# Kernel tuning notes

Hardware: AMD Instinct MI355X
Metric: run time of the kernel (lower is better)

Reference implementation:

```python
import jax, jax.numpy as jnp
import numpy as np

F = 32  # node channels (both convs)


def ecc_conv(x, src, dst, e, fgn_w, fgn_b, root, bias):
    """Edge-conditioned conv: per-edge kernel from edge feats, gather-matmul-scatter."""
    n_nodes = x.shape[0]
    n_edges = e.shape[0]
    f_in = x.shape[1]
    # filter-generating network: (E, S) -> (E, F_in*F_out) -> (E, F_in, F_out)
    kernels = (e @ fgn_w + fgn_b).reshape(n_edges, f_in, F)
    # gather source node feats, per-edge matmul
    messages = jnp.einsum('ef,efo->eo', x[src], kernels)
    # scatter-sum to target nodes
    agg = jax.ops.segment_sum(messages, dst, num_segments=n_nodes)
    return jax.nn.relu(agg + x @ root + bias)


def setup_inputs() -> dict:
    key = jax.random.key(0)
    ks = jax.random.split(key, 12)
    N, E, S = 50000, 200000, 16
    s = 0.05  # small init scale to keep activations bounded through relu
    return {
        'x': jax.random.normal(ks[0], (N, F), jnp.float32),
        'e': jax.random.normal(ks[1], (E, S), jnp.float32),
        'src': jax.random.randint(ks[2], (E,), 0, N, jnp.int32),
        'dst': jax.random.randint(ks[3], (E,), 0, N, jnp.int32),
        'fgn_w1': jax.random.normal(ks[4], (S, F * F), jnp.float32) * s,
        'fgn_b1': jnp.zeros((F * F,), jnp.float32),
        'root1': jax.random.normal(ks[5], (F, F), jnp.float32) * s,
        'bias1': jnp.zeros((F,), jnp.float32),
        'fgn_w2': jax.random.normal(ks[6], (S, F * F), jnp.float32) * s,
        'fgn_b2': jnp.zeros((F * F,), jnp.float32),
        'root2': jax.random.normal(ks[7], (F, F), jnp.float32) * s,
        'bias2': jnp.zeros((F,), jnp.float32),
        'dense_w': jax.random.normal(ks[8], (F, 1), jnp.float32) * s,
        'dense_b': jnp.zeros((1,), jnp.float32),
    }


def reference(x, e, src, dst, fgn_w1, fgn_b1, root1, bias1,
              fgn_w2, fgn_b2, root2, bias2, dense_w, dense_b):
    h = ecc_conv(x, src, dst, e, fgn_w1, fgn_b1, root1, bias1)
    h = ecc_conv(h, src, dst, e, fgn_w2, fgn_b2, root2, bias2)
    pooled = jnp.sum(h, axis=0)          # global sum pool over nodes -> (F,)
    return pooled @ dense_w + dense_b    # (1,)
```

## Files before the change

### kernel.cpp

```cpp
#include <hip/hip_runtime.h>
#include <hip/hip_bf16.h>

#define F 32
#define S 16

typedef short v8s __attribute__((ext_vector_type(8)));
typedef float v4f __attribute__((ext_vector_type(4)));

__device__ __forceinline__ float bf_lo(unsigned u) { return __uint_as_float(u << 16); }
__device__ __forceinline__ float bf_hi(unsigned u) { return __uint_as_float(u & 0xffff0000u); }
__device__ __forceinline__ unsigned short f2bf(float f) {
    __hip_bfloat16 h = __float2bfloat16(f);
    return *(unsigned short*)&h;
}
__device__ __forceinline__ unsigned pack2(float a, float b) {
    return (unsigned)f2bf(a) | ((unsigned)f2bf(b) << 16);
}
static inline size_t align256(size_t b) { return (b + 255) & ~(size_t)255; }

__global__ __launch_bounds__(256) void convert_w2(
    const float* __restrict__ w1, const float* __restrict__ b1, const float* __restrict__ r1,
    const float* __restrict__ w2, const float* __restrict__ b2, const float* __restrict__ r2,
    unsigned short* __restrict__ Wf1, unsigned short* __restrict__ Wf2,
    unsigned short* __restrict__ Rt1, unsigned short* __restrict__ Rt2)
{
    const int PER = 34 * 512 + 32 * 32;
    int tid = blockIdx.x * blockDim.x + threadIdx.x;
    if (tid >= 2 * PER) return;
    const int layer = tid / PER;
    const int rem   = tid % PER;
    const float* w = layer ? w2 : w1;
    const float* b = layer ? b2 : b1;
    const float* r = layer ? r2 : r1;
    if (rem < 34 * 512) {
        const int fi   = rem >> 9;
        const int rr   = rem & 511;
        const int lane = rr >> 3;
        const int j    = rr & 7;
        const int half = fi & 1;
        const int ck   = fi >> 1;
        const int o    = (half << 4) | (lane & 15);
        const int k    = ck * 32 + (lane >> 4) * 8 + j;
        const int s    = k >> 5, f = k & 31;
        const float v  = (s < S) ? w[s * (F * F) + f * F + o] : b[f * F + o];
        (layer ? Wf2 : Wf1)[rem] = f2bf(v);
    } else {
        const int q = rem - 34 * 512;
        const int o = q >> 5, f = q & 31;
        (layer ? Rt2 : Rt1)[o * F + f] = f2bf(r[f * F + o]);
    }
}

__global__ __launch_bounds__(256) void hist_kernel(
    const int* __restrict__ dst, int* __restrict__ cnt, int E)
{
    int e = blockIdx.x * blockDim.x + threadIdx.x;
    if (e < E) atomicAdd(&cnt[dst[e]], 1);
}

__global__ __launch_bounds__(256) void scan_partial(
    const int* __restrict__ cnt, int* __restrict__ partial, int N)
{
    const int i = blockIdx.x * 256 + threadIdx.x;
    int v = (i < N) ? cnt[i] : 0;
    #pragma unroll
    for (int off = 32; off > 0; off >>= 1) v += __shfl_down(v, off, 64);
    __shared__ int wsum[4];
    const int wave = threadIdx.x >> 6, lane = threadIdx.x & 63;
    if (lane == 0) wsum[wave] = v;
    __syncthreads();
    if (threadIdx.x == 0)
        partial[blockIdx.x] = wsum[0] + wsum[1] + wsum[2] + wsum[3];
}

__global__ void scan_top(int* __restrict__ partial, int M)
{
    const int t = threadIdx.x;
    int carry = 0;
    for (int base = 0; base < M; base += 64) {
        const int i = base + t;
        const int v0 = (i < M) ? partial[i] : 0;
        int v = v0;
        #pragma unroll
        for (int off = 1; off < 64; off <<= 1) {
            int u = __shfl_up(v, off, 64);
            if (t >= off) v += u;
        }
        if (i < M) partial[i] = carry + (v - v0);
        carry += __shfl(v, 63, 64);
    }
}

__global__ __launch_bounds__(256) void scan_final(
    const int* __restrict__ cnt, const int* __restrict__ partial,
    int* __restrict__ cursor, int* __restrict__ rowptr, int N)
{
    const int i = blockIdx.x * 256 + threadIdx.x;
    const int v0 = (i < N) ? cnt[i] : 0;
    int v = v0;
    const int wave = threadIdx.x >> 6, lane = threadIdx.x & 63;
    #pragma unroll
    for (int off = 1; off < 64; off <<= 1) {
        int u = __shfl_up(v, off, 64);
        if (lane >= off) v += u;
    }
    __shared__ int wsum[4];
    if (lane == 63) wsum[wave] = v;
    __syncthreads();
    int woff = 0;
    for (int ww = 0; ww < 4; ++ww) woff += (ww < wave) ? wsum[ww] : 0;
    if (i < N) {
        const int excl = partial[blockIdx.x] + woff + (v - v0);
        cursor[i] = excl;
        rowptr[i] = excl;
    }
}

__global__ __launch_bounds__(256) void scatter_kernel(
    const int* __restrict__ dst, int* __restrict__ cursor,
    int* __restrict__ perm, int E)
{
    int e = blockIdx.x * blockDim.x + threadIdx.x;
    if (e < E) {
        int p = atomicAdd(&cursor[dst[e]], 1);
        perm[p] = e;
    }
}

__global__ __launch_bounds__(256) void esort_kernel(
    const float* __restrict__ ef, const int* __restrict__ src,
    const int* __restrict__ perm,
    float* __restrict__ ef_s, int* __restrict__ src_s, int E)
{
    const int gid = blockIdx.x * blockDim.x + threadIdx.x;
    const int slot = gid >> 2;
    if (slot >= E) return;
    const int q = gid & 3;
    const int e = perm[slot];
    ((float4*)(ef_s + (size_t)slot * S))[q] = ((const float4*)(ef + (size_t)e * S))[q];
    if (q == 0) src_s[slot] = src[e];
}

__global__ __launch_bounds__(256) void edge_msg(
    const float* __restrict__ xin,
    const float* __restrict__ ef_s,
    const int* __restrict__ src_s,
    const unsigned short* __restrict__ Wf,
    unsigned short* __restrict__ msg,
    int E)
{
    __shared__ v8s Wl[34 * 64];
    const int tid  = threadIdx.x;
    const int w    = tid >> 6;
    const int lane = tid & 63;
    const int lid  = lane & 15;
    const int quad = lane >> 4;

    {
        const uint4* s = (const uint4*)Wf;
        uint4* d = (uint4*)Wl;
        #pragma unroll
        for (int i = 0; i < 9; ++i) {
            const int idx = tid + 256 * i;
            if (idx < 2176) d[idx] = s[idx];
        }
    }
    __syncthreads();

    const int nTiles = (E + 15) >> 4;
    for (int tile = blockIdx.x * 4 + w; tile < nTiles; tile += gridDim.x * 4) {
        const int  slot = tile * 16 + lid;
        const bool live = (slot < E);
        const int  s    = live ? slot : 0;
        const int  sn   = src_s[s];
        const float4* xp = (const float4*)(xin + (size_t)sn * F + quad * 8);
        const float4 xv0 = xp[0], xv1 = xp[1];
        const float4* efv = (const float4*)(ef_s + (size_t)s * S);
        const float4 c0 = efv[0], c1 = efv[1], c2 = efv[2], c3 = efv[3];
        const float cs[S] = {c0.x, c0.y, c0.z, c0.w, c1.x, c1.y, c1.z, c1.w,
                             c2.x, c2.y, c2.z, c2.w, c3.x, c3.y, c3.z, c3.w};

        v4f acc0 = {0.f, 0.f, 0.f, 0.f};
        v4f acc1 = {0.f, 0.f, 0.f, 0.f};

        #pragma unroll
        for (int ck = 0; ck < S; ++ck) {
            const float sc = cs[ck];
            union { v8s s8; uint4 u4; } fr;
            fr.u4.x = pack2(sc * xv0.x, sc * xv0.y);
            fr.u4.y = pack2(sc * xv0.z, sc * xv0.w);
            fr.u4.z = pack2(sc * xv1.x, sc * xv1.y);
            fr.u4.w = pack2(sc * xv1.z, sc * xv1.w);
            acc0 = __builtin_amdgcn_mfma_f32_16x16x32_bf16(Wl[(2 * ck) * 64 + lane],     fr.s8, acc0, 0, 0, 0);
            acc1 = __builtin_amdgcn_mfma_f32_16x16x32_bf16(Wl[(2 * ck + 1) * 64 + lane], fr.s8, acc1, 0, 0, 0);
        }
        {
            union { v8s s8; uint4 u4; } fr;
            fr.u4.x = pack2(xv0.x, xv0.y);
            fr.u4.y = pack2(xv0.z, xv0.w);
            fr.u4.z = pack2(xv1.x, xv1.y);
            fr.u4.w = pack2(xv1.z, xv1.w);
            acc0 = __builtin_amdgcn_mfma_f32_16x16x32_bf16(Wl[32 * 64 + lane], fr.s8, acc0, 0, 0, 0);
            acc1 = __builtin_amdgcn_mfma_f32_16x16x32_bf16(Wl[33 * 64 + lane], fr.s8, acc1, 0, 0, 0);
        }

        if (live) {
            unsigned short* mp = msg + (size_t)slot * 32;
            uint2 p0, p1;
            p0.x = pack2(acc0[0], acc0[1]);
            p0.y = pack2(acc0[2], acc0[3]);
            p1.x = pack2(acc1[0], acc1[1]);
            p1.y = pack2(acc1[2], acc1[3]);
            *(uint2*)(mp + quad * 4)      = p0;
            *(uint2*)(mp + 16 + quad * 4) = p1;
        }
    }
}

__global__ __launch_bounds__(256) void rootsum(
    const float* __restrict__ in,
    const unsigned short* __restrict__ msg,
    const int* __restrict__ rowptr,
    const int* __restrict__ cnt,
    const unsigned short* __restrict__ Rt,
    const float* __restrict__ bias,
    float* __restrict__ h,
    int N)
{
    __shared__ float acc[64 * 33];
    __shared__ unsigned short As[64 * F];
    const int tid  = threadIdx.x;
    const int n0   = blockIdx.x * 64;
    const int w    = tid >> 6;
    const int lane = tid & 63;
    const int lid  = lane & 15;
    const int quad = lane >> 4;

    {
        const int nl = tid >> 2;
        const int kq = tid & 3;
        int n = n0 + nl; if (n > N - 1) n = N - 1;
        const float4* xp = (const float4*)(in + (size_t)n * F + kq * 8);
        float4 v0 = xp[0], v1 = xp[1];
        uint4 pk;
        pk.x = pack2(v0.x, v0.y);
        pk.y = pack2(v0.z, v0.w);
        pk.z = pack2(v1.x, v1.y);
        pk.w = pack2(v1.z, v1.w);
        const int slot = ((nl >> 4) * 4 + kq) * 16 + (nl & 15);
        *(uint4*)(As + slot * 8) = pk;
    }

    {
        const int nl = tid >> 2;
        const int oq = tid & 3;
        const int n  = n0 + nl;
        float a[8];
        #pragma unroll
        for (int j = 0; j < 8; ++j) a[j] = 0.f;
        if (n < N) {
            const int k0 = rowptr[n];
            const int k1 = k0 + cnt[n];
            for (int k = k0; k < k1; ++k) {
                const uint4 q = *(const uint4*)(msg + (size_t)k * 32 + oq * 8);
                a[0] += bf_lo(q.x); a[1] += bf_hi(q.x);
                a[2] += bf_lo(q.y); a[3] += bf_hi(q.y);
                a[4] += bf_lo(q.z); a[5] += bf_hi(q.z);
                a[6] += bf_lo(q.w); a[7] += bf_hi(q.w);
            }
        }
        float* ap = acc + nl * 33 + oq * 8;
        #pragma unroll
        for (int j = 0; j < 8; ++j) ap[j] = a[j];
    }
    __syncthreads();

    const int jt  = w & 1;
    const int ns0 = (w >> 1) * 2;
    const v8s rf = *(const v8s*)(Rt + (size_t)(jt * 16 + lid) * F + quad * 8);
    const int o0 = jt * 16 + quad * 4;
    const float4 bs = *(const float4*)(bias + o0);

    #pragma unroll
    for (int i = 0; i < 2; ++i) {
        const int ns = ns0 + i;
        const v8s af = *(const v8s*)(As + (((ns * 4 + quad) * 16) + lid) * 8);
        v4f d = {0.f, 0.f, 0.f, 0.f};
        d = __builtin_amdgcn_mfma_f32_16x16x32_bf16(rf, af, d, 0, 0, 0);
        const int n = n0 + ns * 16 + lid;
        if (n < N) {
            const float* ap = acc + (ns * 16 + lid) * 33 + o0;
            float4 hv;
            hv.x = fmaxf(d[0] + ap[0] + bs.x, 0.f);
            hv.y = fmaxf(d[1] + ap[1] + bs.y, 0.f);
            hv.z = fmaxf(d[2] + ap[2] + bs.z, 0.f);
            hv.w = fmaxf(d[3] + ap[3] + bs.w, 0.f);
            *(float4*)(h + (size_t)n * F + o0) = hv;
        }
    }
}

__global__ __launch_bounds__(256) void pool_kernel(
    const float* __restrict__ h, float* __restrict__ pooled, int N)
{
    const int c = threadIdx.x & (F - 1);
    const int rowsPerBlock = 256 / F;
    float p = 0.0f;
    for (int n = blockIdx.x * rowsPerBlock + (threadIdx.x >> 5);
         n < N; n += gridDim.x * rowsPerBlock)
        p += h[(size_t)n * F + c];
    __shared__ float red[256];
    red[threadIdx.x] = p;
    __syncthreads();
    for (int off = 128; off >= F; off >>= 1) {
        if (threadIdx.x < off) red[threadIdx.x] += red[threadIdx.x + off];
        __syncthreads();
    }
    if (threadIdx.x < F) atomicAdd(&pooled[threadIdx.x], red[threadIdx.x]);
}

__global__ void final_kernel(
    const float* __restrict__ pooled, const float* __restrict__ dw,
    const float* __restrict__ db, float* __restrict__ out)
{
    const int o = threadIdx.x;
    float v = (o < F) ? pooled[o] * dw[o] : 0.0f;
    #pragma unroll
    for (int off = 32; off > 0; off >>= 1) v += __shfl_down(v, off, 64);
    if (o == 0) out[0] = v + db[0];
}

__global__ __launch_bounds__(256, 2) void ecc_edge_slow(
    const float* __restrict__ x, const float* __restrict__ ef,
    const int* __restrict__ src, const int* __restrict__ dst,
    const float* __restrict__ W, const float* __restrict__ B,
    float* __restrict__ agg, int E)
{
    const int tid = blockIdx.x * blockDim.x + threadIdx.x;
    const bool live = (tid < E);
    const int e = live ? tid : (E - 1);
    const int sn = src[e], dn = dst[e];
    float xr[F];
    const float4* xp = (const float4*)(x + (size_t)sn * F);
    #pragma unroll
    for (int i = 0; i < F / 4; ++i) {
        float4 v = xp[i];
        xr[4*i+0] = v.x; xr[4*i+1] = v.y; xr[4*i+2] = v.z; xr[4*i+3] = v.w;
    }
    float acc[F];
    #pragma unroll
    for (int o = 0; o < F; ++o) acc[o] = 0.0f;
    const float* erow = ef + (size_t)e * S;
    for (int s = 0; s < S; ++s) {
        const float es = erow[s];
        const float* Ws = W + s * (F * F);
        #pragma unroll
        for (int f = 0; f < F; ++f) {
            const float z = es * xr[f];
            #pragma unroll
            for (int o = 0; o < F; ++o) acc[o] = fmaf(z, Ws[f * F + o], acc[o]);
        }
    }
    #pragma unroll
    for (int f = 0; f < F; ++f) {
        const float xf = xr[f];
        #pragma unroll
        for (int o = 0; o < F; ++o) acc[o] = fmaf(xf, B[f * F + o], acc[o]);
    }
    if (live) {
        float* ap = agg + (size_t)dn * F;
        #pragma unroll
        for (int o = 0; o < F; ++o) atomicAdd(ap + o, acc[o]);
    }
}

__global__ __launch_bounds__(256) void ecc_node_slow(
    const float* __restrict__ xin, const float* __restrict__ root,
    const float* __restrict__ bias, float* __restrict__ h, int N)
{
    int t = blockIdx.x * blockDim.x + threadIdx.x;
    if (t >= N * F) return;
    const int n = t >> 5, o = t & (F - 1);
    const float* xrow = xin + (size_t)n * F;
    float v = h[t] + bias[o];
    #pragma unroll
    for (int f = 0; f < F; ++f) v = fmaf(xrow[f], root[f * F + o], v);
    h[t] = fmaxf(v, 0.0f);
}

extern "C" void kernel_launch(void* const* d_in, const int* in_sizes, int n_in,
                              void* d_out, int out_size, void* d_ws, size_t ws_size,
                              hipStream_t stream) {
    const float* x      = (const float*)d_in[0];
    const float* efeat  = (const float*)d_in[1];
    const int*   src    = (const int*)d_in[2];
    const int*   dst    = (const int*)d_in[3];
    const float* fgn_w1 = (const float*)d_in[4];
    const float* fgn_b1 = (const float*)d_in[5];
    const float* root1  = (const float*)d_in[6];
    const float* bias1  = (const float*)d_in[7];
    const float* fgn_w2 = (const float*)d_in[8];
    const float* fgn_b2 = (const float*)d_in[9];
    const float* root2  = (const float*)d_in[10];
    const float* bias2  = (const float*)d_in[11];
    const float* dense_w = (const float*)d_in[12];
    const float* dense_b = (const float*)d_in[13];

    const int N = in_sizes[0] / F;
    const int E = in_sizes[2];

    const int gridP = (N + 255) / 256;

    const size_t pooledB = 256;
    const size_t cntB    = align256((size_t)N * 4);
    const size_t rowB    = align256((size_t)N * 4);
    const size_t curB    = align256((size_t)N * 4);
    const size_t partB   = align256((size_t)gridP * 4);
    const size_t permB   = align256((size_t)E * 4);
    const size_t efsB    = align256((size_t)E * S * 4);
    const size_t srcsB   = align256((size_t)E * 4);
    const size_t msgB    = align256((size_t)E * 32 * 2);
    const size_t hB      = (size_t)N * F * 4;
    const size_t wfB     = align256((size_t)34 * 512 * 2);
    const size_t rtB     = align256((size_t)32 * 32 * 2);

    const size_t offCnt  = pooledB;
    const size_t offRow  = offCnt + cntB;
    const size_t offCur  = offRow + rowB;
    const size_t offPart = offCur + curB;
    const size_t offPerm = offPart + partB;
    const size_t offEfs  = offPerm + permB;
    const size_t offSrcs = offEfs + efsB;
    const size_t offMsg  = offSrcs + srcsB;
    const size_t offH1   = offMsg + msgB;
    const size_t offH2   = offH1 + hB;
    const size_t offW1   = offH2 + hB;
    const size_t offW2   = offW1 + wfB;
    const size_t offR1   = offW2 + wfB;
    const size_t offR2   = offR1 + rtB;
    const size_t need    = offR2 + rtB;

    const int eB         = (E + 255) / 256;
    const int nodeBlocks = (N * F + 255) / 256;

    if (ws_size >= need) {
        float* pooled = (float*)d_ws;
        int* cnt     = (int*)((char*)d_ws + offCnt);
        int* rowptr  = (int*)((char*)d_ws + offRow);
        int* cursor  = (int*)((char*)d_ws + offCur);
        int* partial = (int*)((char*)d_ws + offPart);
        int* perm    = (int*)((char*)d_ws + offPerm);
        float* ef_s  = (float*)((char*)d_ws + offEfs);
        int*   src_s = (int*)((char*)d_ws + offSrcs);
        unsigned short* msg = (unsigned short*)((char*)d_ws + offMsg);
        float* h1    = (float*)((char*)d_ws + offH1);
        float* h2    = (float*)((char*)d_ws + offH2);
        unsigned short* Wf1 = (unsigned short*)((char*)d_ws + offW1);
        unsigned short* Wf2 = (unsigned short*)((char*)d_ws + offW2);
        unsigned short* Rt1 = (unsigned short*)((char*)d_ws + offR1);
        unsigned short* Rt2 = (unsigned short*)((char*)d_ws + offR2);

        hipMemsetAsync(d_ws, 0, pooledB + cntB, stream);

        convert_w2<<<(2 * 18432 + 255) / 256, 256, 0, stream>>>(
            fgn_w1, fgn_b1, root1, fgn_w2, fgn_b2, root2, Wf1, Wf2, Rt1, Rt2);

        hist_kernel   <<<eB, 256, 0, stream>>>(dst, cnt, E);
        scan_partial  <<<gridP, 256, 0, stream>>>(cnt, partial, N);
        scan_top      <<<1, 64, 0, stream>>>(partial, gridP);
        scan_final    <<<gridP, 256, 0, stream>>>(cnt, partial, cursor, rowptr, N);
        scatter_kernel<<<eB, 256, 0, stream>>>(dst, cursor, perm, E);
        esort_kernel  <<<(E * 4 + 255) / 256, 256, 0, stream>>>(efeat, src, perm, ef_s, src_s, E);

        const int nTiles     = (E + 15) / 16;
        int edgeBlocks = (nTiles + 3) / 4;
        if (edgeBlocks > 1024) edgeBlocks = 1024;
        const int rsBlocks   = (N + 63) / 64;

        edge_msg<<<edgeBlocks, 256, 0, stream>>>(x, ef_s, src_s, Wf1, msg, E);
        rootsum <<<rsBlocks, 256, 0, stream>>>(x, msg, rowptr, cnt, Rt1, bias1, h1, N);

        edge_msg<<<edgeBlocks, 256, 0, stream>>>(h1, ef_s, src_s, Wf2, msg, E);
        rootsum <<<rsBlocks, 256, 0, stream>>>(h1, msg, rowptr, cnt, Rt2, bias2, h2, N);

        pool_kernel <<<512, 256, 0, stream>>>(h2, pooled, N);
        final_kernel<<<1, 64, 0, stream>>>(pooled, dense_w, dense_b, (float*)d_out);
    } else {
        float* agg1   = (float*)d_ws;
        float* agg2   = agg1 + (size_t)N * F;
        float* pooled = agg2 + (size_t)N * F;
        hipMemsetAsync(d_ws, 0, (2 * (size_t)N * F + F) * sizeof(float), stream);
        ecc_edge_slow<<<eB, 256, 0, stream>>>(x, efeat, src, dst, fgn_w1, fgn_b1, agg1, E);
        ecc_node_slow<<<nodeBlocks, 256, 0, stream>>>(x, root1, bias1, agg1, N);
        ecc_edge_slow<<<eB, 256, 0, stream>>>(agg1, efeat, src, dst, fgn_w2, fgn_b2, agg2, E);
        ecc_node_slow<<<nodeBlocks, 256, 0, stream>>>(agg1, root2, bias2, agg2, N);
        pool_kernel <<<512, 256, 0, stream>>>(agg2, pooled, N);
        final_kernel<<<1, 64, 0, stream>>>(pooled, dense_w, dense_b, (float*)d_out);
    }
}
```

Baseline: 203.0 us.

## Fuse edge message MFMA with node aggregation and root transform per node block

```diff
diff --git a/kernel.cpp b/kernel.cpp
--- a/kernel.cpp
+++ b/kernel.cpp
@@ -129,8 +129,9 @@
 
 __global__ __launch_bounds__(256) void esort_kernel(
     const float* __restrict__ ef, const int* __restrict__ src,
-    const int* __restrict__ perm,
-    float* __restrict__ ef_s, int* __restrict__ src_s, int E)
+    const int* __restrict__ dst, const int* __restrict__ perm,
+    float* __restrict__ ef_s, int* __restrict__ src_s, int* __restrict__ dst_s,
+    int E)
 {
     const int gid = blockIdx.x * blockDim.x + threadIdx.x;
     const int slot = gid >> 2;
@@ -139,94 +140,22 @@
     const int e = perm[slot];
     ((float4*)(ef_s + (size_t)slot * S))[q] = ((const float4*)(ef + (size_t)e * S))[q];
     if (q == 0) src_s[slot] = src[e];
-}
-
-__global__ __launch_bounds__(256) void edge_msg(
-    const float* __restrict__ xin,
+    if (q == 1) dst_s[slot] = dst[e];
+}
+
+__global__ __launch_bounds__(256) void ecc_fused(
+    const float* __restrict__ in,
     const float* __restrict__ ef_s,
     const int* __restrict__ src_s,
+    const int* __restrict__ dst_s,
+    const int* __restrict__ rowptr,
     const unsigned short* __restrict__ Wf,
-    unsigned short* __restrict__ msg,
-    int E)
-{
-    __shared__ v8s Wl[34 * 64];
-    const int tid  = threadIdx.x;
-    const int w    = tid >> 6;
-    const int lane = tid & 63;
-    const int lid  = lane & 15;
-    const int quad = lane >> 4;
-
-    {
-        const uint4* s = (const uint4*)Wf;
-        uint4* d = (uint4*)Wl;
-        #pragma unroll
-        for (int i = 0; i < 9; ++i) {
-            const int idx = tid + 256 * i;
-            if (idx < 2176) d[idx] = s[idx];
-        }
-    }
-    __syncthreads();
-
-    const int nTiles = (E + 15) >> 4;
-    for (int tile = blockIdx.x * 4 + w; tile < nTiles; tile += gridDim.x * 4) {
-        const int  slot = tile * 16 + lid;
-        const bool live = (slot < E);
-        const int  s    = live ? slot : 0;
-        const int  sn   = src_s[s];
-        const float4* xp = (const float4*)(xin + (size_t)sn * F + quad * 8);
-        const float4 xv0 = xp[0], xv1 = xp[1];
-        const float4* efv = (const float4*)(ef_s + (size_t)s * S);
-        const float4 c0 = efv[0], c1 = efv[1], c2 = efv[2], c3 = efv[3];
-        const float cs[S] = {c0.x, c0.y, c0.z, c0.w, c1.x, c1.y, c1.z, c1.w,
-                             c2.x, c2.y, c2.z, c2.w, c3.x, c3.y, c3.z, c3.w};
-
-        v4f acc0 = {0.f, 0.f, 0.f, 0.f};
-        v4f acc1 = {0.f, 0.f, 0.f, 0.f};
-
-        #pragma unroll
-        for (int ck = 0; ck < S; ++ck) {
-            const float sc = cs[ck];
-            union { v8s s8; uint4 u4; } fr;
-            fr.u4.x = pack2(sc * xv0.x, sc * xv0.y);
-            fr.u4.y = pack2(sc * xv0.z, sc * xv0.w);
-            fr.u4.z = pack2(sc * xv1.x, sc * xv1.y);
-            fr.u4.w = pack2(sc * xv1.z, sc * xv1.w);
-            acc0 = __builtin_amdgcn_mfma_f32_16x16x32_bf16(Wl[(2 * ck) * 64 + lane],     fr.s8, acc0, 0, 0, 0);
-            acc1 = __builtin_amdgcn_mfma_f32_16x16x32_bf16(Wl[(2 * ck + 1) * 64 + lane], fr.s8, acc1, 0, 0, 0);
-        }
-        {
-            union { v8s s8; uint4 u4; } fr;
-            fr.u4.x = pack2(xv0.x, xv0.y);
-            fr.u4.y = pack2(xv0.z, xv0.w);
-            fr.u4.z = pack2(xv1.x, xv1.y);
-            fr.u4.w = pack2(xv1.z, xv1.w);
-            acc0 = __builtin_amdgcn_mfma_f32_16x16x32_bf16(Wl[32 * 64 + lane], fr.s8, acc0, 0, 0, 0);
-            acc1 = __builtin_amdgcn_mfma_f32_16x16x32_bf16(Wl[33 * 64 + lane], fr.s8, acc1, 0, 0, 0);
-        }
-
-        if (live) {
-            unsigned short* mp = msg + (size_t)slot * 32;
-            uint2 p0, p1;
-            p0.x = pack2(acc0[0], acc0[1]);
-            p0.y = pack2(acc0[2], acc0[3]);
-            p1.x = pack2(acc1[0], acc1[1]);
-            p1.y = pack2(acc1[2], acc1[3]);
-            *(uint2*)(mp + quad * 4)      = p0;
-            *(uint2*)(mp + 16 + quad * 4) = p1;
-        }
-    }
-}
-
-__global__ __launch_bounds__(256) void rootsum(
-    const float* __restrict__ in,
-    const unsigned short* __restrict__ msg,
-    const int* __restrict__ rowptr,
-    const int* __restrict__ cnt,
     const unsigned short* __restrict__ Rt,
     const float* __restrict__ bias,
     float* __restrict__ h,
-    int N)
-{
+    int N, int E)
+{
+    __shared__ v8s Wl[34 * 64];
     __shared__ float acc[64 * 33];
     __shared__ unsigned short As[64 * F];
     const int tid  = threadIdx.x;
@@ -236,6 +165,17 @@
     const int lid  = lane & 15;
     const int quad = lane >> 4;
 
+    {
+        const uint4* s = (const uint4*)Wf;
+        uint4* d = (uint4*)Wl;
+        #pragma unroll
+        for (int i = 0; i < 9; ++i) {
+            const int idx = tid + 256 * i;
+            if (idx < 2176) d[idx] = s[idx];
+        }
+    }
+    #pragma unroll
+    for (int i = tid; i < 64 * 33; i += 256) acc[i] = 0.f;
     {
         const int nl = tid >> 2;
         const int kq = tid & 3;
@@ -250,28 +190,52 @@
         const int slot = ((nl >> 4) * 4 + kq) * 16 + (nl & 15);
         *(uint4*)(As + slot * 8) = pk;
     }
-
-    {
-        const int nl = tid >> 2;
-        const int oq = tid & 3;
-        const int n  = n0 + nl;
-        float a[8];
-        #pragma unroll
-        for (int j = 0; j < 8; ++j) a[j] = 0.f;
-        if (n < N) {
-            const int k0 = rowptr[n];
-            const int k1 = k0 + cnt[n];
-            for (int k = k0; k < k1; ++k) {
-                const uint4 q = *(const uint4*)(msg + (size_t)k * 32 + oq * 8);
-                a[0] += bf_lo(q.x); a[1] += bf_hi(q.x);
-                a[2] += bf_lo(q.y); a[3] += bf_hi(q.y);
-                a[4] += bf_lo(q.z); a[5] += bf_hi(q.z);
-                a[6] += bf_lo(q.w); a[7] += bf_hi(q.w);
-            }
-        }
-        float* ap = acc + nl * 33 + oq * 8;
-        #pragma unroll
-        for (int j = 0; j < 8; ++j) ap[j] = a[j];
+    __syncthreads();
+
+    const int half = w & 1;
+    const int k0   = rowptr[n0];
+    const int kEnd = (n0 + 64 < N) ? rowptr[n0 + 64] : E;
+
+    for (int k = k0 + (w >> 1) * 16; k < kEnd; k += 32) {
+        const int  slot = k + lid;
+        const bool live = (slot < kEnd);
+        const int  sl   = live ? slot : k;
+        const int  sn   = src_s[sl];
+        const int  dn   = dst_s[sl];
+        const float4* xp = (const float4*)(in + (size_t)sn * F + quad * 8);
+        const float4 xv0 = xp[0], xv1 = xp[1];
+        const float4* efv = (const float4*)(ef_s + (size_t)sl * S);
+        const float4 c0 = efv[0], c1 = efv[1], c2 = efv[2], c3 = efv[3];
+        const float cs[S] = {c0.x, c0.y, c0.z, c0.w, c1.x, c1.y, c1.z, c1.w,
+                             c2.x, c2.y, c2.z, c2.w, c3.x, c3.y, c3.z, c3.w};
+
+        v4f a = {0.f, 0.f, 0.f, 0.f};
+        #pragma unroll
+        for (int ck = 0; ck < S; ++ck) {
+            const float sc = cs[ck];
+            union { v8s s8; uint4 u4; } fr;
+            fr.u4.x = pack2(sc * xv0.x, sc * xv0.y);
+            fr.u4.y = pack2(sc * xv0.z, sc * xv0.w);
+            fr.u4.z = pack2(sc * xv1.x, sc * xv1.y);
+            fr.u4.w = pack2(sc * xv1.z, sc * xv1.w);
+            a = __builtin_amdgcn_mfma_f32_16x16x32_bf16(Wl[(2 * ck + half) * 64 + lane], fr.s8, a, 0, 0, 0);
+        }
+        {
+            union { v8s s8; uint4 u4; } fr;
+            fr.u4.x = pack2(xv0.x, xv0.y);
+            fr.u4.y = pack2(xv0.z, xv0.w);
+            fr.u4.z = pack2(xv1.x, xv1.y);
+            fr.u4.w = pack2(xv1.z, xv1.w);
+            a = __builtin_amdgcn_mfma_f32_16x16x32_bf16(Wl[(32 + half) * 64 + lane], fr.s8, a, 0, 0, 0);
+        }
+
+        if (live) {
+            float* ap = acc + (dn - n0) * 33 + half * 16 + quad * 4;
+            atomicAdd(ap + 0, a[0]);
+            atomicAdd(ap + 1, a[1]);
+            atomicAdd(ap + 2, a[2]);
+            atomicAdd(ap + 3, a[3]);
+        }
     }
     __syncthreads();
 
@@ -419,7 +383,7 @@
     const size_t permB   = align256((size_t)E * 4);
     const size_t efsB    = align256((size_t)E * S * 4);
     const size_t srcsB   = align256((size_t)E * 4);
-    const size_t msgB    = align256((size_t)E * 32 * 2);
+    const size_t dstsB   = align256((size_t)E * 4);
     const size_t hB      = (size_t)N * F * 4;
     const size_t wfB     = align256((size_t)34 * 512 * 2);
     const size_t rtB     = align256((size_t)32 * 32 * 2);
@@ -431,8 +395,8 @@
     const size_t offPerm = offPart + partB;
     const size_t offEfs  = offPerm + permB;
     const size_t offSrcs = offEfs + efsB;
-    const size_t offMsg  = offSrcs + srcsB;
-    const size_t offH1   = offMsg + msgB;
+    const size_t offDsts = offSrcs + srcsB;
+    const size_t offH1   = offDsts + dstsB;
     const size_t offH2   = offH1 + hB;
     const size_t offW1   = offH2 + hB;
     const size_t offW2   = offW1 + wfB;
@@ -452,7 +416,7 @@
         int* perm    = (int*)((char*)d_ws + offPerm);
         float* ef_s  = (float*)((char*)d_ws + offEfs);
         int*   src_s = (int*)((char*)d_ws + offSrcs);
-        unsigned short* msg = (unsigned short*)((char*)d_ws + offMsg);
+        int*   dst_s = (int*)((char*)d_ws + offDsts);
         float* h1    = (float*)((char*)d_ws + offH1);
         float* h2    = (float*)((char*)d_ws + offH2);
         unsigned short* Wf1 = (unsigned short*)((char*)d_ws + offW1);
@@ -470,18 +434,15 @@
         scan_top      <<<1, 64, 0, stream>>>(partial, gridP);
         scan_final    <<<gridP, 256, 0, stream>>>(cnt, partial, cursor, rowptr, N);
         scatter_kernel<<<eB, 256, 0, stream>>>(dst, cursor, perm, E);
-        esort_kernel  <<<(E * 4 + 255) / 256, 256, 0, stream>>>(efeat, src, perm, ef_s, src_s, E);
-
-        const int nTiles     = (E + 15) / 16;
-        int edgeBlocks = (nTiles + 3) / 4;
-        if (edgeBlocks > 1024) edgeBlocks = 1024;
-        const int rsBlocks   = (N + 63) / 64;
-
-        edge_msg<<<edgeBlocks, 256, 0, stream>>>(x, ef_s, src_s, Wf1, msg, E);
-        rootsum <<<rsBlocks, 256, 0, stream>>>(x, msg, rowptr, cnt, Rt1, bias1, h1, N);
-
-        edge_msg<<<edgeBlocks, 256, 0, stream>>>(h1, ef_s, src_s, Wf2, msg, E);
-        rootsum <<<rsBlocks, 256, 0, stream>>>(h1, msg, rowptr, cnt, Rt2, bias2, h2, N);
+        esort_kernel  <<<(E * 4 + 255) / 256, 256, 0, stream>>>(
+            efeat, src, dst, perm, ef_s, src_s, dst_s, E);
+
+        const int layerBlocks = (N + 63) / 64;
+
+        ecc_fused<<<layerBlocks, 256, 0, stream>>>(
+            x,  ef_s, src_s, dst_s, rowptr, Wf1, Rt1, bias1, h1, N, E);
+        ecc_fused<<<layerBlocks, 256, 0, stream>>>(
+            h1, ef_s, src_s, dst_s, rowptr, Wf2, Rt2, bias2, h2, N, E);
 
         pool_kernel <<<512, 256, 0, stream>>>(h2, pooled, N);
         final_kernel<<<1, 64, 0, stream>>>(pooled, dense_w, dense_b, (float*)d_out);
```

Measured after the change: 269.0 us. 1.32x slower.

## Fuse preprocessing and pooling kernels to cut launch count and perm buffer

Applied to the files above, without the earlier changes.

```diff
diff --git a/kernel.cpp b/kernel.cpp
--- a/kernel.cpp
+++ b/kernel.cpp
@@ -18,44 +18,40 @@
 }
 static inline size_t align256(size_t b) { return (b + 255) & ~(size_t)255; }
 
-__global__ __launch_bounds__(256) void convert_w2(
+__global__ __launch_bounds__(256) void conv_hist(
     const float* __restrict__ w1, const float* __restrict__ b1, const float* __restrict__ r1,
     const float* __restrict__ w2, const float* __restrict__ b2, const float* __restrict__ r2,
     unsigned short* __restrict__ Wf1, unsigned short* __restrict__ Wf2,
-    unsigned short* __restrict__ Rt1, unsigned short* __restrict__ Rt2)
+    unsigned short* __restrict__ Rt1, unsigned short* __restrict__ Rt2,
+    const int* __restrict__ dst, int* __restrict__ cnt, int E)
 {
     const int PER = 34 * 512 + 32 * 32;
-    int tid = blockIdx.x * blockDim.x + threadIdx.x;
-    if (tid >= 2 * PER) return;
-    const int layer = tid / PER;
-    const int rem   = tid % PER;
-    const float* w = layer ? w2 : w1;
-    const float* b = layer ? b2 : b1;
-    const float* r = layer ? r2 : r1;
-    if (rem < 34 * 512) {
-        const int fi   = rem >> 9;
-        const int rr   = rem & 511;
-        const int lane = rr >> 3;
-        const int j    = rr & 7;
-        const int half = fi & 1;
-        const int ck   = fi >> 1;
-        const int o    = (half << 4) | (lane & 15);
-        const int k    = ck * 32 + (lane >> 4) * 8 + j;
-        const int s    = k >> 5, f = k & 31;
-        const float v  = (s < S) ? w[s * (F * F) + f * F + o] : b[f * F + o];
-        (layer ? Wf2 : Wf1)[rem] = f2bf(v);
-    } else {
-        const int q = rem - 34 * 512;
-        const int o = q >> 5, f = q & 31;
-        (layer ? Rt2 : Rt1)[o * F + f] = f2bf(r[f * F + o]);
-    }
-}
-
-__global__ __launch_bounds__(256) void hist_kernel(
-    const int* __restrict__ dst, int* __restrict__ cnt, int E)
-{
-    int e = blockIdx.x * blockDim.x + threadIdx.x;
-    if (e < E) atomicAdd(&cnt[dst[e]], 1);
+    const int tid = blockIdx.x * blockDim.x + threadIdx.x;
+    if (tid < 2 * PER) {
+        const int layer = tid / PER;
+        const int rem   = tid % PER;
+        const float* w = layer ? w2 : w1;
+        const float* b = layer ? b2 : b1;
+        const float* r = layer ? r2 : r1;
+        if (rem < 34 * 512) {
+            const int fi   = rem >> 9;
+            const int rr   = rem & 511;
+            const int lane = rr >> 3;
+            const int j    = rr & 7;
+            const int half = fi & 1;
+            const int ck   = fi >> 1;
+            const int o    = (half << 4) | (lane & 15);
+            const int k    = ck * 32 + (lane >> 4) * 8 + j;
+            const int s    = k >> 5, f = k & 31;
+            const float v  = (s < S) ? w[s * (F * F) + f * F + o] : b[f * F + o];
+            (layer ? Wf2 : Wf1)[rem] = f2bf(v);
+        } else {
+            const int q = rem - 34 * 512;
+            const int o = q >> 5, f = q & 31;
+            (layer ? Rt2 : Rt1)[o * F + f] = f2bf(r[f * F + o]);
+        }
+    }
+    if (tid < E) atomicAdd(&cnt[dst[tid]], 1);
 }
 
 __global__ __launch_bounds__(256) void scan_partial(
@@ -73,28 +69,21 @@
         partial[blockIdx.x] = wsum[0] + wsum[1] + wsum[2] + wsum[3];
 }
 
-__global__ void scan_top(int* __restrict__ partial, int M)
-{
-    const int t = threadIdx.x;
-    int carry = 0;
-    for (int base = 0; base < M; base += 64) {
-        const int i = base + t;
-        const int v0 = (i < M) ? partial[i] : 0;
-        int v = v0;
-        #pragma unroll
-        for (int off = 1; off < 64; off <<= 1) {
-            int u = __shfl_up(v, off, 64);
-            if (t >= off) v += u;
-        }
-        if (i < M) partial[i] = carry + (v - v0);
-        carry += __shfl(v, 63, 64);
-    }
-}
-
 __global__ __launch_bounds__(256) void scan_final(
     const int* __restrict__ cnt, const int* __restrict__ partial,
     int* __restrict__ cursor, int* __restrict__ rowptr, int N)
 {
+    __shared__ int redI[256];
+    int b = 0;
+    for (int j = threadIdx.x; j < blockIdx.x; j += 256) b += partial[j];
+    redI[threadIdx.x] = b;
+    __syncthreads();
+    for (int off = 128; off >= 1; off >>= 1) {
+        if (threadIdx.x < off) redI[threadIdx.x] += redI[threadIdx.x + off];
+        __syncthreads();
+    }
+    const int base = redI[0];
+
     const int i = blockIdx.x * 256 + threadIdx.x;
     const int v0 = (i < N) ? cnt[i] : 0;
     int v = v0;
@@ -110,35 +99,24 @@
     int woff = 0;
     for (int ww = 0; ww < 4; ++ww) woff += (ww < wave) ? wsum[ww] : 0;
     if (i < N) {
-        const int excl = partial[blockIdx.x] + woff + (v - v0);
+        const int excl = base + woff + (v - v0);
         cursor[i] = excl;
         rowptr[i] = excl;
     }
 }
 
-__global__ __launch_bounds__(256) void scatter_kernel(
+__global__ __launch_bounds__(256) void scatter_sort(
+    const float* __restrict__ ef, const int* __restrict__ src,
     const int* __restrict__ dst, int* __restrict__ cursor,
-    int* __restrict__ perm, int E)
-{
-    int e = blockIdx.x * blockDim.x + threadIdx.x;
-    if (e < E) {
-        int p = atomicAdd(&cursor[dst[e]], 1);
-        perm[p] = e;
-    }
-}
-
-__global__ __launch_bounds__(256) void esort_kernel(
-    const float* __restrict__ ef, const int* __restrict__ src,
-    const int* __restrict__ perm,
     float* __restrict__ ef_s, int* __restrict__ src_s, int E)
 {
-    const int gid = blockIdx.x * blockDim.x + threadIdx.x;
-    const int slot = gid >> 2;
-    if (slot >= E) return;
-    const int q = gid & 3;
-    const int e = perm[slot];
-    ((float4*)(ef_s + (size_t)slot * S))[q] = ((const float4*)(ef + (size_t)e * S))[q];
-    if (q == 0) src_s[slot] = src[e];
+    const int e = blockIdx.x * blockDim.x + threadIdx.x;
+    if (e >= E) return;
+    const int p = atomicAdd(&cursor[dst[e]], 1);
+    src_s[p] = src[e];
+    const float4* s = (const float4*)(ef + (size_t)e * S);
+    float4* d = (float4*)(ef_s + (size_t)p * S);
+    d[0] = s[0]; d[1] = s[1]; d[2] = s[2]; d[3] = s[3];
 }
 
 __global__ __launch_bounds__(256) void edge_msg(
@@ -300,14 +278,14 @@
     }
 }
 
-__global__ __launch_bounds__(256) void pool_kernel(
-    const float* __restrict__ h, float* __restrict__ pooled, int N)
+__global__ __launch_bounds__(256) void pool_final(
+    const float* __restrict__ h, float* __restrict__ pooled, int* __restrict__ counter,
+    const float* __restrict__ dw, const float* __restrict__ db,
+    float* __restrict__ out, int N, int nBlocks)
 {
     const int c = threadIdx.x & (F - 1);
-    const int rowsPerBlock = 256 / F;
     float p = 0.0f;
-    for (int n = blockIdx.x * rowsPerBlock + (threadIdx.x >> 5);
-         n < N; n += gridDim.x * rowsPerBlock)
+    for (int n = blockIdx.x * 8 + (threadIdx.x >> 5); n < N; n += gridDim.x * 8)
         p += h[(size_t)n * F + c];
     __shared__ float red[256];
     red[threadIdx.x] = p;
@@ -317,17 +295,21 @@
         __syncthreads();
     }
     if (threadIdx.x < F) atomicAdd(&pooled[threadIdx.x], red[threadIdx.x]);
-}
-
-__global__ void final_kernel(
-    const float* __restrict__ pooled, const float* __restrict__ dw,
-    const float* __restrict__ db, float* __restrict__ out)
-{
-    const int o = threadIdx.x;
-    float v = (o < F) ? pooled[o] * dw[o] : 0.0f;
-    #pragma unroll
-    for (int off = 32; off > 0; off >>= 1) v += __shfl_down(v, off, 64);
-    if (o == 0) out[0] = v + db[0];
+    __threadfence();
+    __shared__ int lastFlag;
+    if (threadIdx.x == 0) {
+        const int t = atomicAdd(counter, 1);
+        lastFlag = (t == nBlocks - 1) ? 1 : 0;
+    }
+    __syncthreads();
+    if (lastFlag && threadIdx.x < 64) {
+        const int o = threadIdx.x;
+        float v = 0.f;
+        if (o < F) v = atomicAdd(&pooled[o], 0.0f) * dw[o];
+        #pragma unroll
+        for (int off = 32; off > 0; off >>= 1) v += __shfl_down(v, off, 64);
+        if (o == 0) out[0] = v + db[0];
+    }
 }
 
 __global__ __launch_bounds__(256, 2) void ecc_edge_slow(
@@ -386,6 +368,34 @@
     #pragma unroll
     for (int f = 0; f < F; ++f) v = fmaf(xrow[f], root[f * F + o], v);
     h[t] = fmaxf(v, 0.0f);
+}
+
+__global__ __launch_bounds__(256) void pool_kernel(
+    const float* __restrict__ h, float* __restrict__ pooled, int N)
+{
+    const int c = threadIdx.x & (F - 1);
+    float p = 0.0f;
+    for (int n = blockIdx.x * 8 + (threadIdx.x >> 5); n < N; n += gridDim.x * 8)
+        p += h[(size_t)n * F + c];
+    __shared__ float red[256];
+    red[threadIdx.x] = p;
+    __syncthreads();
+    for (int off = 128; off >= F; off >>= 1) {
+        if (threadIdx.x < off) red[threadIdx.x] += red[threadIdx.x + off];
+        __syncthreads();
+    }
+    if (threadIdx.x < F) atomicAdd(&pooled[threadIdx.x], red[threadIdx.x]);
+}
+
+__global__ void final_kernel(
+    const float* __restrict__ pooled, const float* __restrict__ dw,
+    const float* __restrict__ db, float* __restrict__ out)
+{
+    const int o = threadIdx.x;
+    float v = (o < F) ? pooled[o] * dw[o] : 0.0f;
+    #pragma unroll
+    for (int off = 32; off > 0; off >>= 1) v += __shfl_down(v, off, 64);
+    if (o == 0) out[0] = v + db[0];
 }
 
 extern "C" void kernel_launch(void* const* d_in, const int* in_sizes, int n_in,
@@ -416,7 +426,6 @@
     const size_t rowB    = align256((size_t)N * 4);
     const size_t curB    = align256((size_t)N * 4);
     const size_t partB   = align256((size_t)gridP * 4);
-    const size_t permB   = align256((size_t)E * 4);
     const size_t efsB    = align256((size_t)E * S * 4);
     const size_t srcsB   = align256((size_t)E * 4);
     const size_t msgB    = align256((size_t)E * 32 * 2);
@@ -428,8 +437,7 @@
     const size_t offRow  = offCnt + cntB;
     const size_t offCur  = offRow + rowB;
     const size_t offPart = offCur + curB;
-    const size_t offPerm = offPart + partB;
-    const size_t offEfs  = offPerm + permB;
+    const size_t offEfs  = offPart + partB;
     const size_t offSrcs = offEfs + efsB;
     const size_t offMsg  = offSrcs + srcsB;
     const size_t offH1   = offMsg + msgB;
@@ -444,12 +452,12 @@
     const int nodeBlocks = (N * F + 255) / 256;
 
     if (ws_size >= need) {
-        float* pooled = (float*)d_ws;
+        float* pooled  = (float*)d_ws;
+        int*   counter = (int*)((char*)d_ws + F * sizeof(float));
         int* cnt     = (int*)((char*)d_ws + offCnt);
         int* rowptr  = (int*)((char*)d_ws + offRow);
         int* cursor  = (int*)((char*)d_ws + offCur);
         int* partial = (int*)((char*)d_ws + offPart);
-        int* perm    = (int*)((char*)d_ws + offPerm);
         float* ef_s  = (float*)((char*)d_ws + offEfs);
         int*   src_s = (int*)((char*)d_ws + offSrcs);
         unsigned short* msg = (unsigned short*)((char*)d_ws + offMsg);
@@ -462,15 +470,15 @@
 
         hipMemsetAsync(d_ws, 0, pooledB + cntB, stream);
 
-        convert_w2<<<(2 * 18432 + 255) / 256, 256, 0, stream>>>(
-            fgn_w1, fgn_b1, root1, fgn_w2, fgn_b2, root2, Wf1, Wf2, Rt1, Rt2);
-
-        hist_kernel   <<<eB, 256, 0, stream>>>(dst, cnt, E);
-        scan_partial  <<<gridP, 256, 0, stream>>>(cnt, partial, N);
-        scan_top      <<<1, 64, 0, stream>>>(partial, gridP);
-        scan_final    <<<gridP, 256, 0, stream>>>(cnt, partial, cursor, rowptr, N);
-        scatter_kernel<<<eB, 256, 0, stream>>>(dst, cursor, perm, E);
-        esort_kernel  <<<(E * 4 + 255) / 256, 256, 0, stream>>>(efeat, src, perm, ef_s, src_s, E);
+        const int chBlocks = (E > 2 * 18432 ? E : 2 * 18432);
+        conv_hist<<<(chBlocks + 255) / 256, 256, 0, stream>>>(
+            fgn_w1, fgn_b1, root1, fgn_w2, fgn_b2, root2,
+            Wf1, Wf2, Rt1, Rt2, dst, cnt, E);
+
+        scan_partial<<<gridP, 256, 0, stream>>>(cnt, partial, N);
+        scan_final  <<<gridP, 256, 0, stream>>>(cnt, partial, cursor, rowptr, N);
+
+        scatter_sort<<<eB, 256, 0, stream>>>(efeat, src, dst, cursor, ef_s, src_s, E);
 
         const int nTiles     = (E + 15) / 16;
         int edgeBlocks = (nTiles + 3) / 4;
@@ -483,8 +491,8 @@
         edge_msg<<<edgeBlocks, 256, 0, stream>>>(h1, ef_s, src_s, Wf2, msg, E);
         rootsum <<<rsBlocks, 256, 0, stream>>>(h1, msg, rowptr, cnt, Rt2, bias2, h2, N);
 
-        pool_kernel <<<512, 256, 0, stream>>>(h2, pooled, N);
-        final_kernel<<<1, 64, 0, stream>>>(pooled, dense_w, dense_b, (float*)d_out);
+        pool_final<<<512, 256, 0, stream>>>(h2, pooled, counter, dense_w, dense_b,
+                                            (float*)d_out, N, 512);
     } else {
         float* agg1   = (float*)d_ws;
         float* agg2   = agg1 + (size_t)N * F;
```

Measured after the change: 214.0 us. +5.4%, slower.
